# Performance work log

Hardware: AMD Instinct MI355X
Metric: run time of the kernel (lower is better)

Reference implementation:

```python
import jax, jax.numpy as jnp
import numpy as np

B, S, E, D = 8, 2048, 1024, 128  # batch, seq (== max_span), embed_size, att_block_size


def setup_inputs() -> dict:
    key = jax.random.key(0)
    kx, kq, kk, kv = jax.random.split(key, 4)
    x = jax.random.normal(kx, (B, S, E), dtype=jnp.float32)
    # torch nn.Linear weight layout: [out_features, in_features]
    scale = 1.0 / np.sqrt(E)
    Wq = jax.random.normal(kq, (D, E), dtype=jnp.float32) * scale
    Wk = jax.random.normal(kk, (D, E), dtype=jnp.float32) * scale
    Wv = jax.random.normal(kv, (D, E), dtype=jnp.float32) * scale
    return {"x": x, "Wq": Wq, "Wk": Wk, "Wv": Wv}


def reference(x, Wq, Wk, Wv):
    # q/k/v projections: nn.Linear without bias -> x @ W.T
    q = jnp.einsum('bse,de->bsd', x, Wq)  # [B,S,D]
    k = jnp.einsum('bse,de->bsd', x, Wk)
    v = jnp.einsum('bse,de->bsd', x, Wv)

    scores = jnp.einsum('bqd,bkd->bqk', q, k)  # [B,S,S]
    # causal mask (tril): -inf above diagonal
    causal = jnp.tril(jnp.ones((S, S), dtype=bool))
    scores = jnp.where(causal, scores, -jnp.inf)
    # faithful to source: scores divided by sqrt(D) TWICE => effective 1/D
    scores = scores / jnp.float32(D)
    attn = jax.nn.softmax(scores, axis=-1)
    z = jnp.einsum('bqk,bkd->bqd', attn, v)  # [B,S,D]
    return z
```

## Files before the change

kernel.cpp:

```cpp
#include <hip/hip_runtime.h>
#include <cstdint>
#include <cstddef>

#define DEV __device__ __forceinline__

typedef float  f32x4  __attribute__((ext_vector_type(4)));
typedef __bf16 bf16x4 __attribute__((ext_vector_type(4)));
typedef __bf16 bf16x8 __attribute__((ext_vector_type(8)));

constexpr int B = 8, S = 2048, E = 1024, D = 128;
constexpr int M = B * S;

constexpr size_t WS_QKV   = (size_t)3 * M * D;
constexpr size_t WS_NEED  = (WS_QKV + (size_t)3 * D * E) * 2;

DEV int sniff_is_bf16(const uint32_t* w) {
  int lane = threadIdx.x & 63;
  uint32_t v = w[lane * 1001];
  int e = (v >> 7) & 0xff;
  unsigned long long b = __ballot(e >= 100 && e <= 140);
  return __popcll(b) >= 48;
}

DEV bf16x4 cvt4(float4 f) {
  bf16x4 r; r[0] = (__bf16)f.x; r[1] = (__bf16)f.y; r[2] = (__bf16)f.z; r[3] = (__bf16)f.w;
  return r;
}

DEV void glds16(const void* g, void* l) {
  __builtin_amdgcn_global_load_lds(
      (const __attribute__((address_space(1))) void*)g,
      (__attribute__((address_space(3))) void*)l, 16, 0, 0);
}

__global__ __launch_bounds__(256) void wcast_kernel(
    const void* __restrict__ xp, const void* __restrict__ wqp,
    const void* __restrict__ wkp, const void* __restrict__ wvp,
    unsigned short* __restrict__ wbf) {
  const int is_b = sniff_is_bf16((const uint32_t*)xp);
  const int row = blockIdx.x;
  const void* src = row < 128 ? wqp : (row < 256 ? wkp : wvp);
  const int r = row & 127;
  const int t = threadIdx.x;
  if (is_b) {
    const uint2* s = (const uint2*)((const unsigned short*)src + (size_t)r * E) + t;
    *((uint2*)(wbf + (size_t)row * E) + t) = *s;
  } else {
    float4 f = *((const float4*)((const float*)src + (size_t)r * E) + t);
    *((bf16x4*)(wbf + (size_t)row * E) + t) = cvt4(f);
  }
}

__global__ __launch_bounds__(512, 4) void proj_kernel(
    const void* __restrict__ xp, const void* __restrict__ wqp,
    const void* __restrict__ wkp, const void* __restrict__ wvp,
    const unsigned short* __restrict__ wbf, const int use_wbf,
    unsigned short* __restrict__ ws) {
  __shared__ __align__(16) unsigned short lds[(32 + 384) * 72];
  unsigned short* xbuf = lds;
  unsigned short* wbuf = lds + 32 * 72;

  const int is_b = sniff_is_bf16((const uint32_t*)xp);
  const int m0 = blockIdx.x * 32;

  const int t = threadIdx.x, lane = t & 63, w = t >> 6;
  const int n15 = lane & 15, quad = lane >> 4;
  const int rg = w >> 2, cg = w & 3;

  f32x4 acc[6] = {};
  const int sr = t >> 3, sc8 = (t & 7) * 8;
  const int wr = t >> 3;

  for (int it = 0; it < 16; ++it) {
    const int k0 = it * 64;
    __syncthreads();
    if (t < 256) {
      if (!is_b) {
        const float4* sx = (const float4*)((const float*)xp + (size_t)(m0 + sr) * E + k0 + sc8);
        *(bf16x4*)&xbuf[sr * 72 + sc8] = cvt4(sx[0]);
        *(bf16x4*)&xbuf[sr * 72 + sc8 + 4] = cvt4(sx[1]);
      } else {
        *(uint4*)&xbuf[sr * 72 + sc8] =
            *(const uint4*)((const unsigned short*)xp + (size_t)(m0 + sr) * E + k0 + sc8);
      }
    }
    if (use_wbf) {
#pragma unroll
      for (int j = 0; j < 6; ++j)
        *(uint4*)&wbuf[(j * 64 + wr) * 72 + sc8] =
            *(const uint4*)(wbf + (size_t)(j * 64 + wr) * E + k0 + sc8);
    } else if (!is_b) {
#pragma unroll
      for (int j = 0; j < 6; ++j) {
        const float* wsrc = (j < 2) ? (const float*)wqp : (j < 4) ? (const float*)wkp : (const float*)wvp;
        const int wrow = (j & 1) * 64 + wr;
        const float4* sw = (const float4*)(wsrc + (size_t)wrow * E + k0 + sc8);
        *(bf16x4*)&wbuf[(j * 64 + wr) * 72 + sc8] = cvt4(sw[0]);
        *(bf16x4*)&wbuf[(j * 64 + wr) * 72 + sc8 + 4] = cvt4(sw[1]);
      }
    } else {
#pragma unroll
      for (int j = 0; j < 6; ++j) {
        const unsigned short* wsrc = (j < 2) ? (const unsigned short*)wqp
                                   : (j < 4) ? (const unsigned short*)wkp
                                             : (const unsigned short*)wvp;
        const int wrow = (j & 1) * 64 + wr;
        *(uint4*)&wbuf[(j * 64 + wr) * 72 + sc8] =
            *(const uint4*)(wsrc + (size_t)wrow * E + k0 + sc8);
      }
    }
    __syncthreads();
#pragma unroll
    for (int ks = 0; ks < 2; ++ks) {
      bf16x8 a = *(const bf16x8*)&xbuf[(rg * 16 + n15) * 72 + ks * 32 + quad * 8];
#pragma unroll
      for (int nf = 0; nf < 6; ++nf) {
        bf16x8 bfr = *(const bf16x8*)&wbuf[(cg * 96 + nf * 16 + n15) * 72 + ks * 32 + quad * 8];
        acc[nf] = __builtin_amdgcn_mfma_f32_16x16x32_bf16(a, bfr, acc[nf], 0, 0, 0);
      }
    }
  }

  unsigned short* qws = ws;
  unsigned short* kws = ws + (size_t)M * D;
  unsigned short* vtw = ws + (size_t)2 * M * D;

  __syncthreads();
  unsigned short* tbuf = lds;
#pragma unroll
  for (int nf = 0; nf < 6; ++nf) {
    const int col = cg * 96 + nf * 16 + n15;
    const int self = col >> 7;
    if (self < 2) {
      unsigned short* dst = self ? kws : qws;
      const int gcol = col & 127;
#pragma unroll
      for (int rr = 0; rr < 4; ++rr) {
        const int grow = m0 + rg * 16 + quad * 4 + rr;
        ((__bf16*)dst)[(size_t)grow * D + gcol] = (__bf16)acc[nf][rr];
      }
    } else {
      const int vcol = col - 256;
#pragma unroll
      for (int rr = 0; rr < 4; ++rr)
        ((__bf16*)tbuf)[(rg * 16 + quad * 4 + rr) * 132 + vcol] = (__bf16)acc[nf][rr];
    }
  }
  __syncthreads();
  {
    const int dcol = t >> 2, mst = (t & 3) * 8;
    unsigned short tmp[8] __attribute__((aligned(16)));
#pragma unroll
    for (int j = 0; j < 8; ++j) tmp[j] = tbuf[(mst + j) * 132 + dcol];
    *(uint4*)&vtw[(size_t)dcol * M + m0 + mst] = *(const uint4*)&tmp[0];
  }
}

__global__ __launch_bounds__(256, 2) void attn_kernel(
    const void* __restrict__ xp, const unsigned short* __restrict__ ws,
    void* __restrict__ outp) {
  __shared__ __align__(16) unsigned short kvbuf[2 * 16384];
  __shared__ __align__(16) unsigned short ldsP[4 * 640];
  __shared__ float lbuf[32];
  __shared__ int cnt2[2];

  const int is_b = sniff_is_bf16((const uint32_t*)xp);
  const int bx = blockIdx.x;
  const int batch = bx & 7;
  const int g8 = (bx & 255) >> 3;
  const int t16 = (bx < 256) ? (63 - g8) : g8;
  const int q0 = t16 * 32;
  const int t = threadIdx.x, lane = t & 63, s = t >> 6;
  const int qg = s >> 1, kh = s & 1;
  const int n15 = lane & 15, quad = lane >> 4;

  const unsigned short* qws = ws;
  const unsigned short* kws = ws + (size_t)M * D;
  const unsigned short* vtw = ws + (size_t)2 * M * D;
  unsigned short* ldsPw = ldsP + s * 640;

  if (t < 2) cnt2[t] = 0;

  bf16x8 qf[4];
  {
    const size_t qbase = (size_t)(batch * S + q0 + qg * 16 + n15) * D;
#pragma unroll
    for (int ks = 0; ks < 4; ++ks)
      qf[ks] = *(const bf16x8*)&qws[qbase + ks * 32 + quad * 8];
  }

  const bf16x8 ones = {(__bf16)1.0f, (__bf16)1.0f, (__bf16)1.0f, (__bf16)1.0f,
                       (__bf16)1.0f, (__bf16)1.0f, (__bf16)1.0f, (__bf16)1.0f};

  f32x4 o[8] = {};
  f32x4 lacc = {};

  const int nch = (q0 + 95) >> 6;
  const int wrow = q0 + qg * 16 + 15;
  const int ncw = (wrow >= kh * 32) ? (((wrow - kh * 32) >> 6) + 1) : 0;

  const int r4 = lane >> 4, c16 = lane & 15;
  const int r8 = lane >> 3, c8 = lane & 7;
  const size_t kgbase = (size_t)(batch * S) * D;
  const size_t vgbase = (size_t)batch * S;

#define STAGE(j0c, b)                                                            \
  {                                                                              \
    unsigned short* kb_ = kvbuf + (b)*16384;                                     \
    unsigned short* vb_ = kb_ + 8192;                                            \
    _Pragma("unroll") for (int j = 0; j < 4; ++j) {                              \
      const int krow = s * 16 + j * 4 + r4;                 \
      glds16(kws + kgbase + (size_t)((j0c) + krow) * D + ((c16 ^ (krow & 7)) << 3), \
             kb_ + (s * 16 + j * 4) * 128);                                      \
    }                                                                            \
    _Pragma("unroll") for (int j = 0; j < 4; ++j) {                              \
      const int dr = s * 32 + j * 8 + r8;                      \
      glds16(vtw + (size_t)dr * M + vgbase + (j0c) + ((c8 ^ (dr & 7)) << 3),     \
             vb_ + (s * 32 + j * 8) * 64);                                       \
    }                                                                            \
  }

  STAGE(0, 0);

  for (int c = 0; c < nch; ++c) {
    if (c + 1 < nch) {
      STAGE((c + 1) * 64, (c + 1) & 1);
      asm volatile("s_waitcnt vmcnt(8)" ::: "memory");
    } else {
      asm volatile("s_waitcnt vmcnt(0)" ::: "memory");
    }
    __builtin_amdgcn_s_barrier();

    if (c < ncw) {
      const unsigned short* kb = kvbuf + (c & 1) * 16384;
      const unsigned short* vb = kb + 8192;
      const int xsw = n15 & 7;

      f32x4 sc[2] = {};
      __builtin_amdgcn_s_setprio(1);
#pragma unroll
      for (int nt = 0; nt < 2; ++nt) {
        const int klrow = kh * 32 + nt * 16 + n15;
#pragma unroll
        for (int ks = 0; ks < 4; ++ks) {
          const bf16x8 ka = *(const bf16x8*)&kb[klrow * 128 + (((ks * 4 + quad) ^ xsw) << 3)];
          sc[nt] = __builtin_amdgcn_mfma_f32_16x16x32_bf16(ka, qf[ks], sc[nt], 0, 0, 0);
        }
      }
      __builtin_amdgcn_s_setprio(0);

      const int j0 = c * 64 + kh * 32;
      const bool maskc = (c == ncw - 1);
#pragma unroll
      for (int nt = 0; nt < 2; ++nt) {
        bf16x4 pv;
#pragma unroll
        for (int rr = 0; rr < 4; ++rr) {
          float v = sc[nt][rr] * (1.0f / 128.0f);
          if (maskc && (j0 + nt * 16 + quad * 4 + rr > q0 + qg * 16 + n15)) v = -1e30f;
          pv[rr] = (__bf16)__expf(v);
        }
        *(bf16x4*)&ldsPw[n15 * 40 + nt * 16 + quad * 4] = pv;
      }

      const bf16x8 pa = *(const bf16x8*)&ldsPw[n15 * 40 + quad * 8];
      __builtin_amdgcn_s_setprio(1);
#pragma unroll
      for (int dn = 0; dn < 8; ++dn) {
        const bf16x8 vfr =
            *(const bf16x8*)&vb[(dn * 16 + n15) * 64 + (((kh * 4 + quad) ^ xsw) << 3)];
        o[dn] = __builtin_amdgcn_mfma_f32_16x16x32_bf16(pa, vfr, o[dn], 0, 0, 0);
      }
      lacc = __builtin_amdgcn_mfma_f32_16x16x32_bf16(pa, ones, lacc, 0, 0, 0);
      __builtin_amdgcn_s_setprio(0);
    }

    __builtin_amdgcn_s_barrier();
  }

  __syncthreads();

  float* Obuf = (float*)kvbuf;
  if (kh == 0) {
#pragma unroll
    for (int dn = 0; dn < 8; ++dn)
#pragma unroll
      for (int rr = 0; rr < 4; ++rr)
        Obuf[(qg * 16 + quad * 4 + rr) * 132 + dn * 16 + n15] = o[dn][rr];
    if (n15 == 0)
#pragma unroll
      for (int rr = 0; rr < 4; ++rr)
        lbuf[qg * 16 + quad * 4 + rr] = lacc[rr];
    asm volatile("" ::: "memory");
    if (lane == 0) atomicAdd(&cnt2[qg], 1);
  } else {
    while (__hip_atomic_load(&cnt2[qg], __ATOMIC_RELAXED, __HIP_MEMORY_SCOPE_WORKGROUP) < 1)
      __builtin_amdgcn_s_sleep(1);
    asm volatile("" ::: "memory");
#pragma unroll
    for (int dn = 0; dn < 8; ++dn)
#pragma unroll
      for (int rr = 0; rr < 4; ++rr)
        atomicAdd(&Obuf[(qg * 16 + quad * 4 + rr) * 132 + dn * 16 + n15], o[dn][rr]);
    if (n15 == 0)
#pragma unroll
      for (int rr = 0; rr < 4; ++rr)
        atomicAdd(&lbuf[qg * 16 + quad * 4 + rr], lacc[rr]);
    if (lane == 0) atomicAdd(&cnt2[qg], 1);
  }
  while (__hip_atomic_load(&cnt2[0], __ATOMIC_RELAXED, __HIP_MEMORY_SCOPE_WORKGROUP) < 2 ||
         __hip_atomic_load(&cnt2[1], __ATOMIC_RELAXED, __HIP_MEMORY_SCOPE_WORKGROUP) < 2)
    __builtin_amdgcn_s_sleep(1);
  asm volatile("" ::: "memory");

  {
    const int row = t >> 3, cb = (t & 7) * 16;
    const float invl = 1.0f / lbuf[row];
    const size_t grow = (size_t)(batch * S + q0 + row) * D;
    if (is_b) {
#pragma unroll
      for (int i = 0; i < 16; ++i)
        ((__bf16*)outp)[grow + cb + i] = (__bf16)(Obuf[row * 132 + cb + i] * invl);
    } else {
#pragma unroll
      for (int i = 0; i < 16; ++i)
        ((float*)outp)[grow + cb + i] = Obuf[row * 132 + cb + i] * invl;
    }
  }
#undef STAGE
}

extern "C" void kernel_launch(void* const* d_in, const int* in_sizes, int n_in,
                              void* d_out, int out_size, void* d_ws, size_t ws_size,
                              hipStream_t stream) {
  (void)in_sizes; (void)n_in; (void)out_size;
  const void* x  = d_in[0];
  const void* wq = d_in[1];
  const void* wk = d_in[2];
  const void* wv = d_in[3];
  unsigned short* ws = (unsigned short*)d_ws;
  unsigned short* wbf = ws + WS_QKV;
  const int use_wbf = (ws_size >= WS_NEED) ? 1 : 0;

  if (use_wbf)
    wcast_kernel<<<dim3(384), dim3(256), 0, stream>>>(x, wq, wk, wv, wbf);
  proj_kernel<<<dim3(512), dim3(512), 0, stream>>>(x, wq, wk, wv, wbf, use_wbf, ws);
  attn_kernel<<<dim3(512), dim3(256), 0, stream>>>(x, ws, d_out);
}
```

Before: 172.9 us.

## Split causal attention key range into two segments merged via fp32 atomics

Adds a split-K style attention kernel where each query tile's key chunks are divided into two segments handled by separate blocks, doubling the grid to 1024 blocks. Partial unnormalized outputs and row sums are accumulated with global fp32 atomics into a workspace that the weight-cast kernel zeroes first, and a new finalize kernel divides by the row sum and writes the output. This targets load imbalance and low occupancy from long causal tiles, at the cost of atomic traffic, an extra 8MB fp32 buffer to zero and read back, and an additional launch. It is only taken when the workspace is large enough.

Result: no change. 174.8 us (+1.1%).

```diff
diff --git a/kernel.cpp b/kernel.cpp
--- a/kernel.cpp
+++ b/kernel.cpp
@@ -11,8 +11,11 @@
 constexpr int B = 8, S = 2048, E = 1024, D = 128;
 constexpr int M = B * S;
 
-constexpr size_t WS_QKV   = (size_t)3 * M * D;
-constexpr size_t WS_NEED  = (WS_QKV + (size_t)3 * D * E) * 2;
+constexpr size_t WS_QKV    = (size_t)3 * M * D;
+constexpr size_t WS_F32OFF = WS_QKV + (size_t)3 * D * E;
+constexpr size_t WS_NEED   = WS_F32OFF * 2;
+constexpr size_t WS_NEED2  = WS_F32OFF * 2 + ((size_t)M * D + M) * 4;
+constexpr int    NZ4       = (M * D + M) / 4;
 
 DEV int sniff_is_bf16(const uint32_t* w) {
   int lane = threadIdx.x & 63;
@@ -36,7 +39,7 @@
 __global__ __launch_bounds__(256) void wcast_kernel(
     const void* __restrict__ xp, const void* __restrict__ wqp,
     const void* __restrict__ wkp, const void* __restrict__ wvp,
-    unsigned short* __restrict__ wbf) {
+    unsigned short* __restrict__ wbf, float* __restrict__ zbuf, const int nz4) {
   const int is_b = sniff_is_bf16((const uint32_t*)xp);
   const int row = blockIdx.x;
   const void* src = row < 128 ? wqp : (row < 256 ? wkp : wvp);
@@ -49,6 +52,11 @@
     float4 f = *((const float4*)((const float*)src + (size_t)r * E) + t);
     *((bf16x4*)(wbf + (size_t)row * E) + t) = cvt4(f);
   }
+  if (nz4) {
+    float4 z = {0.f, 0.f, 0.f, 0.f};
+    float4* zp = (float4*)zbuf;
+    for (int i = blockIdx.x * 256 + t; i < nz4; i += 384 * 256) zp[i] = z;
+  }
 }
 
 __global__ __launch_bounds__(512, 4) void proj_kernel(
@@ -156,6 +164,141 @@
   }
 }
 
+__global__ __launch_bounds__(256, 2) void attn_seg_kernel(
+    const unsigned short* __restrict__ ws, float* __restrict__ ws2,
+    float* __restrict__ lws) {
+  __shared__ __align__(16) unsigned short kvbuf[2 * 16384];
+  __shared__ __align__(16) unsigned short ldsP[4 * 640];
+
+  const int bx = blockIdx.x;
+  const int batch = bx & 7;
+  const int seg = (bx >> 3) & 1;
+  const int t16 = 63 - (bx >> 4);
+  const int q0 = t16 * 32;
+
+  const int nch = (q0 + 95) >> 6;
+  const int c0 = seg ? ((nch + 1) >> 1) : 0;
+  const int c1 = seg ? nch : ((nch + 1) >> 1);
+  if (c0 >= c1) return;
+
+  const int t = threadIdx.x, lane = t & 63, s = t >> 6;
+  const int qg = s >> 1, kh = s & 1;
+  const int n15 = lane & 15, quad = lane >> 4;
+
+  const unsigned short* qws = ws;
+  const unsigned short* kws = ws + (size_t)M * D;
+  const unsigned short* vtw = ws + (size_t)2 * M * D;
+  unsigned short* ldsPw = ldsP + s * 640;
+
+  bf16x8 qf[4];
+  {
+    const size_t qbase = (size_t)(batch * S + q0 + qg * 16 + n15) * D;
+#pragma unroll
+    for (int ks = 0; ks < 4; ++ks)
+      qf[ks] = *(const bf16x8*)&qws[qbase + ks * 32 + quad * 8];
+  }
+
+  const bf16x8 ones = {(__bf16)1.0f, (__bf16)1.0f, (__bf16)1.0f, (__bf16)1.0f,
+                       (__bf16)1.0f, (__bf16)1.0f, (__bf16)1.0f, (__bf16)1.0f};
+
+  f32x4 o[8] = {};
+  f32x4 lacc = {};
+
+  const int wrow = q0 + qg * 16 + 15;
+  const int ncw = (wrow >= kh * 32) ? (((wrow - kh * 32) >> 6) + 1) : 0;
+
+  const int r4 = lane >> 4, c16 = lane & 15;
+  const int r8 = lane >> 3, c8 = lane & 7;
+  const size_t kgbase = (size_t)(batch * S) * D;
+  const size_t vgbase = (size_t)batch * S;
+
+#define STAGE(j0c, b)                                                            \
+  {                                                                              \
+    unsigned short* kb_ = kvbuf + (b)*16384;                                     \
+    unsigned short* vb_ = kb_ + 8192;                                            \
+    _Pragma("unroll") for (int j = 0; j < 4; ++j) {                              \
+      const int krow = s * 16 + j * 4 + r4;                                      \
+      glds16(kws + kgbase + (size_t)((j0c) + krow) * D + ((c16 ^ (krow & 7)) << 3), \
+             kb_ + (s * 16 + j * 4) * 128);                                      \
+    }                                                                            \
+    _Pragma("unroll") for (int j = 0; j < 4; ++j) {                              \
+      const int dr = s * 32 + j * 8 + r8;                                        \
+      glds16(vtw + (size_t)dr * M + vgbase + (j0c) + ((c8 ^ (dr & 7)) << 3),     \
+             vb_ + (s * 32 + j * 8) * 64);                                       \
+    }                                                                            \
+  }
+
+  STAGE(c0 * 64, c0 & 1);
+
+  for (int c = c0; c < c1; ++c) {
+    if (c + 1 < c1) {
+      STAGE((c + 1) * 64, (c + 1) & 1);
+      asm volatile("s_waitcnt vmcnt(8)" ::: "memory");
+    } else {
+      asm volatile("s_waitcnt vmcnt(0)" ::: "memory");
+    }
+    __builtin_amdgcn_s_barrier();
+
+    if (c < ncw) {
+      const unsigned short* kb = kvbuf + (c & 1) * 16384;
+      const unsigned short* vb = kb + 8192;
+      const int xsw = n15 & 7;
+
+      f32x4 sc[2] = {};
+      __builtin_amdgcn_s_setprio(1);
+#pragma unroll
+      for (int nt = 0; nt < 2; ++nt) {
+        const int klrow = kh * 32 + nt * 16 + n15;
+#pragma unroll
+        for (int ks = 0; ks < 4; ++ks) {
+          const bf16x8 ka = *(const bf16x8*)&kb[klrow * 128 + (((ks * 4 + quad) ^ xsw) << 3)];
+          sc[nt] = __builtin_amdgcn_mfma_f32_16x16x32_bf16(ka, qf[ks], sc[nt], 0, 0, 0);
+        }
+      }
+      __builtin_amdgcn_s_setprio(0);
+
+      const int j0 = c * 64 + kh * 32;
+      const bool maskc = (c == ncw - 1);
+#pragma unroll
+      for (int nt = 0; nt < 2; ++nt) {
+        bf16x4 pv;
+#pragma unroll
+        for (int rr = 0; rr < 4; ++rr) {
+          float v = sc[nt][rr] * (1.0f / 128.0f);
+          if (maskc && (j0 + nt * 16 + quad * 4 + rr > q0 + qg * 16 + n15)) v = -1e30f;
+          pv[rr] = (__bf16)__expf(v);
+        }
+        *(bf16x4*)&ldsPw[n15 * 40 + nt * 16 + quad * 4] = pv;
+      }
+
+      const bf16x8 pa = *(const bf16x8*)&ldsPw[n15 * 40 + quad * 8];
+      __builtin_amdgcn_s_setprio(1);
+#pragma unroll
+      for (int dn = 0; dn < 8; ++dn) {
+        const bf16x8 vfr =
+            *(const bf16x8*)&vb[(dn * 16 + n15) * 64 + (((kh * 4 + quad) ^ xsw) << 3)];
+        o[dn] = __builtin_amdgcn_mfma_f32_16x16x32_bf16(pa, vfr, o[dn], 0, 0, 0);
+      }
+      lacc = __builtin_amdgcn_mfma_f32_16x16x32_bf16(pa, ones, lacc, 0, 0, 0);
+      __builtin_amdgcn_s_setprio(0);
+    }
+
+    __builtin_amdgcn_s_barrier();
+  }
+#undef STAGE
+
+  float* obase = ws2 + (size_t)(batch * S + q0) * D;
+#pragma unroll
+  for (int dn = 0; dn < 8; ++dn)
+#pragma unroll
+    for (int rr = 0; rr < 4; ++rr)
+      atomicAdd(&obase[(size_t)(qg * 16 + quad * 4 + rr) * D + dn * 16 + n15], o[dn][rr]);
+  if (n15 == 0)
+#pragma unroll
+    for (int rr = 0; rr < 4; ++rr)
+      atomicAdd(&lws[batch * S + q0 + qg * 16 + quad * 4 + rr], lacc[rr]);
+}
+
 __global__ __launch_bounds__(256, 2) void attn_kernel(
     const void* __restrict__ xp, const unsigned short* __restrict__ ws,
     void* __restrict__ outp) {
@@ -209,12 +352,12 @@
     unsigned short* kb_ = kvbuf + (b)*16384;                                     \
     unsigned short* vb_ = kb_ + 8192;                                            \
     _Pragma("unroll") for (int j = 0; j < 4; ++j) {                              \
-      const int krow = s * 16 + j * 4 + r4;                 \
+      const int krow = s * 16 + j * 4 + r4;                                      \
       glds16(kws + kgbase + (size_t)((j0c) + krow) * D + ((c16 ^ (krow & 7)) << 3), \
              kb_ + (s * 16 + j * 4) * 128);                                      \
     }                                                                            \
     _Pragma("unroll") for (int j = 0; j < 4; ++j) {                              \
-      const int dr = s * 32 + j * 8 + r8;                      \
+      const int dr = s * 32 + j * 8 + r8;                                        \
       glds16(vtw + (size_t)dr * M + vgbase + (j0c) + ((c8 ^ (dr & 7)) << 3),     \
              vb_ + (s * 32 + j * 8) * 64);                                       \
     }                                                                            \
@@ -277,6 +420,7 @@
 
     __builtin_amdgcn_s_barrier();
   }
+#undef STAGE
 
   __syncthreads();
 
@@ -327,7 +471,30 @@
         ((float*)outp)[grow + cb + i] = Obuf[row * 132 + cb + i] * invl;
     }
   }
-#undef STAGE
+}
+
+__global__ __launch_bounds__(256) void finalize_kernel(
+    const void* __restrict__ xp, const float* __restrict__ ws2,
+    const float* __restrict__ lws, void* __restrict__ outp) {
+  const int is_b = sniff_is_bf16((const uint32_t*)xp);
+  const size_t g = ((size_t)blockIdx.x * 256 + threadIdx.x) * 8;
+  const int m = (int)(g >> 7);
+  const float invl = 1.0f / lws[m];
+  float4 a = *(const float4*)(ws2 + g);
+  float4 b2 = *(const float4*)(ws2 + g + 4);
+  if (is_b) {
+    bf16x8 r;
+    r[0] = (__bf16)(a.x * invl);  r[1] = (__bf16)(a.y * invl);
+    r[2] = (__bf16)(a.z * invl);  r[3] = (__bf16)(a.w * invl);
+    r[4] = (__bf16)(b2.x * invl); r[5] = (__bf16)(b2.y * invl);
+    r[6] = (__bf16)(b2.z * invl); r[7] = (__bf16)(b2.w * invl);
+    *(bf16x8*)((__bf16*)outp + g) = r;
+  } else {
+    float4 ra = {a.x * invl, a.y * invl, a.z * invl, a.w * invl};
+    float4 rb = {b2.x * invl, b2.y * invl, b2.z * invl, b2.w * invl};
+    *(float4*)((float*)outp + g) = ra;
+    *(float4*)((float*)outp + g + 4) = rb;
+  }
 }
 
 extern "C" void kernel_launch(void* const* d_in, const int* in_sizes, int n_in,
@@ -340,10 +507,19 @@
   const void* wv = d_in[3];
   unsigned short* ws = (unsigned short*)d_ws;
   unsigned short* wbf = ws + WS_QKV;
+  float* ws2 = (float*)(ws + WS_F32OFF);
+  float* lws = ws2 + (size_t)M * D;
   const int use_wbf = (ws_size >= WS_NEED) ? 1 : 0;
+  const int use_seg = (ws_size >= WS_NEED2) ? 1 : 0;
 
   if (use_wbf)
-    wcast_kernel<<<dim3(384), dim3(256), 0, stream>>>(x, wq, wk, wv, wbf);
+    wcast_kernel<<<dim3(384), dim3(256), 0, stream>>>(x, wq, wk, wv, wbf, ws2,
+                                                      use_seg ? NZ4 : 0);
   proj_kernel<<<dim3(512), dim3(512), 0, stream>>>(x, wq, wk, wv, wbf, use_wbf, ws);
-  attn_kernel<<<dim3(512), dim3(256), 0, stream>>>(x, ws, d_out);
-}
+  if (use_seg) {
+    attn_seg_kernel<<<dim3(1024), dim3(256), 0, stream>>>(ws, ws2, lws);
+    finalize_kernel<<<dim3(1024), dim3(256), 0, stream>>>(x, ws2, lws, d_out);
+  } else {
+    attn_kernel<<<dim3(512), dim3(256), 0, stream>>>(x, ws, d_out);
+  }
+}
```
